# Kernel optimization log

Measured on AMD Instinct MI355X. Metric: run time of the kernel, lower is better.

## Reference

```python
import jax, jax.numpy as jnp
import numpy as np

T, H, I, E, TOPK = 4096, 2048, 2048, 16, 2

def setup_inputs() -> dict:
    key = jax.random.key(0)
    k1, k2, k3, k4 = jax.random.split(key, 4)
    return {
        "x": jax.random.normal(k1, (T, H), dtype=jnp.float32),
        "gate_w": jax.random.normal(k2, (E, H), dtype=jnp.float32) * 0.02,
        "ws": jax.random.normal(k3, (E, 2 * I, H), dtype=jnp.float32) * 0.02,
        "w2s": jax.random.normal(k4, (E, H, I), dtype=jnp.float32) * 0.02,
        "top_k": TOPK,
    }

def reference(x, gate_w, ws, w2s, top_k):
    # Router: logits -> softmax -> topk -> renormalize (top_k > 1), per fused_topk.
    logits = x @ gate_w.T                      # [T, E]
    scores = jax.nn.softmax(logits, axis=-1)
    topk_w, topk_ids = jax.lax.top_k(scores, top_k)  # [T, K]
    if top_k > 1:
        topk_w = topk_w / jnp.sum(topk_w, axis=-1, keepdims=True)
    n_exp, two_i, _ = ws.shape
    i_dim = two_i // 2

    def expert_step(acc, inp):
        w13_e, w2_e, e = inp               # [2I,H], [H,I], scalar
        gate_up = x @ w13_e.T              # [T, 2I]
        g, u = gate_up[:, :i_dim], gate_up[:, i_dim:]
        h = jax.nn.silu(g) * u             # SiluAndMul
        y = h @ w2_e.T                     # [T, H]
        coef = jnp.sum(jnp.where(topk_ids == e, topk_w, 0.0), axis=-1)  # [T]
        return acc + coef[:, None] * y, None

    init = jnp.zeros_like(x)
    eids = jnp.arange(n_exp, dtype=topk_ids.dtype)
    out, _ = jax.lax.scan(expert_step, init, (ws, w2s, eids))
    return out
```

## Files before the change

kernel.cpp:

```cpp
#include <hip/hip_runtime.h>
#include <hip/hip_bf16.h>

#define T_DIM 4096
#define H_DIM 2048
#define I_DIM 2048
#define E_NUM 16

#define BM 128
#define BN 128
#define BK 32

#define MAX_ROWS 10240

using frag_ab = __attribute__((ext_vector_type(8))) short;
using frag_cd = __attribute__((ext_vector_type(4))) float;
using ushort8 = __attribute__((ext_vector_type(8))) unsigned short;

__device__ __forceinline__ unsigned short f2bf(float f) {
    unsigned int u = __float_as_uint(f);
    u += 0x7fff + ((u >> 16) & 1);
    return (unsigned short)(u >> 16);
}
__device__ __forceinline__ float bf2f(unsigned short s) {
    return __uint_as_float(((unsigned int)s) << 16);
}

__device__ __forceinline__ void gld16(const void* g, void* l) {
    __builtin_amdgcn_global_load_lds(
        (const __attribute__((address_space(1))) unsigned int*)g,
        (__attribute__((address_space(3))) unsigned int*)l, 16, 0, 0);
}

__global__ void routing_kernel(const float* __restrict__ x,
                               const float* __restrict__ gw,
                               int* __restrict__ cnt,
                               int* __restrict__ tok_list,
                               float* __restrict__ tok_w) {
    const int wave = threadIdx.x >> 6;
    const int lane = threadIdx.x & 63;
    const int t = blockIdx.x * 4 + wave;
    if (t >= T_DIM) return;

    float acc[E_NUM];
#pragma unroll
    for (int e = 0; e < E_NUM; ++e) acc[e] = 0.f;
    const float* xr = x + (size_t)t * H_DIM;
    for (int j = lane; j < H_DIM; j += 64) {
        float xv = xr[j];
#pragma unroll
        for (int e = 0; e < E_NUM; ++e)
            acc[e] = fmaf(xv, gw[e * H_DIM + j], acc[e]);
    }
#pragma unroll
    for (int e = 0; e < E_NUM; ++e) {
        float v = acc[e];
#pragma unroll
        for (int off = 32; off > 0; off >>= 1) v += __shfl_xor(v, off);
        acc[e] = v;
    }
    if (lane == 0) {
        int b1 = 0; float l1 = acc[0];
#pragma unroll
        for (int e = 1; e < E_NUM; ++e)
            if (acc[e] > l1) { l1 = acc[e]; b1 = e; }
        int b2 = -1; float l2 = -1e30f;
#pragma unroll
        for (int e = 0; e < E_NUM; ++e)
            if (e != b1 && acc[e] > l2) { l2 = acc[e]; b2 = e; }
        float w1 = 1.f / (1.f + __expf(l2 - l1));
        float w2 = 1.f - w1;
        int p1 = atomicAdd(&cnt[b1], 1);
        tok_list[b1 * T_DIM + p1] = t; tok_w[b1 * T_DIM + p1] = w1;
        int p2 = atomicAdd(&cnt[b2], 1);
        tok_list[b2 * T_DIM + p2] = t; tok_w[b2 * T_DIM + p2] = w2;
    }
}

__global__ void scan_kernel(const int* __restrict__ cnt, int* __restrict__ base,
                            int* __restrict__ npad, int* __restrict__ total) {
    int acc = 0;
    for (int e = 0; e < E_NUM; ++e) {
        base[e] = acc;
        int p = (cnt[e] + BM - 1) & ~(BM - 1);
        npad[e] = p;
        acc += p;
    }
    *total = acc;
}

__global__ void __launch_bounds__(256) cvt_kernel(const float* __restrict__ s,
                                                  unsigned short* __restrict__ d,
                                                  size_t n8) {
    const size_t stride = (size_t)gridDim.x * 256;
    for (size_t i = (size_t)blockIdx.x * 256 + threadIdx.x; i < n8; i += stride) {
        const float4* sp = (const float4*)(s + i * 8);
        float4 a = sp[0], b = sp[1];
        ushort8 o;
        o[0] = f2bf(a.x); o[1] = f2bf(a.y); o[2] = f2bf(a.z); o[3] = f2bf(a.w);
        o[4] = f2bf(b.x); o[5] = f2bf(b.y); o[6] = f2bf(b.z); o[7] = f2bf(b.w);
        *(ushort8*)(d + i * 8) = o;
    }
}

__global__ void __launch_bounds__(256) gemm1_bf_kernel(
    const unsigned short* __restrict__ xb, const unsigned short* __restrict__ wb,
    const int* __restrict__ tok_list,
    const int* __restrict__ cnt, const int* __restrict__ base,
    const int* __restrict__ npad, unsigned short* __restrict__ gu)
{
    const int e = blockIdx.z;
    const int mt = blockIdx.y;
    if (mt * BM >= npad[e]) return;
    const int nt = blockIdx.x;

    __shared__ unsigned short As[BM * BK];
    __shared__ unsigned short Bs[BN * BK];

    const int tid = threadIdx.x;
    const int lane = tid & 63;
    const int wv = tid >> 6;
    const int wm = (wv >> 1) * 64;
    const int wn = (wv & 1) * 64;
    const int quad = lane >> 4;
    const int l16 = lane & 15;

    const int* tl = tok_list + e * T_DIM + mt * BM;
    const int lim = cnt[e] - mt * BM - 1;

    const int srow = wv * 16 + (lane >> 2);
    const int scol = (lane & 3) * 8;

    const int r0 = srow      <= lim ? srow      : lim;
    const int r1 = srow + 64 <= lim ? srow + 64 : lim;
    const unsigned short* ag0 = xb + (size_t)tl[r0] * H_DIM + scol;
    const unsigned short* ag1 = xb + (size_t)tl[r1] * H_DIM + scol;
    const unsigned short* bg0 = wb + (size_t)e * (2 * I_DIM) * H_DIM
                                   + (size_t)(nt * BN + srow) * H_DIM + scol;
    const unsigned short* bg1 = bg0 + (size_t)64 * H_DIM;

    unsigned short* al0 = &As[wv * 512];
    unsigned short* al1 = &As[2048 + wv * 512];
    unsigned short* bl0 = &Bs[wv * 512];
    unsigned short* bl1 = &Bs[2048 + wv * 512];

    frag_cd acc[4][4];
#pragma unroll
    for (int i = 0; i < 4; ++i)
#pragma unroll
        for (int j = 0; j < 4; ++j)
            acc[i][j] = (frag_cd){0.f, 0.f, 0.f, 0.f};

    for (int k0 = 0; k0 < H_DIM; k0 += BK) {
        gld16(ag0 + k0, al0);
        gld16(ag1 + k0, al1);
        gld16(bg0 + k0, bl0);
        gld16(bg1 + k0, bl1);
        __syncthreads();
        frag_ab af[4], bf[4];
#pragma unroll
        for (int i = 0; i < 4; ++i) {
            af[i] = *(const frag_ab*)(&As[(wm + i * 16 + l16) * BK + quad * 8]);
            bf[i] = *(const frag_ab*)(&Bs[(wn + i * 16 + l16) * BK + quad * 8]);
        }
#pragma unroll
        for (int i = 0; i < 4; ++i)
#pragma unroll
            for (int j = 0; j < 4; ++j)
                acc[i][j] = __builtin_amdgcn_mfma_f32_16x16x32_bf16(
                    af[i], bf[j], acc[i][j], 0, 0, 0);
        __syncthreads();
    }

    const size_t gbase = (size_t)(base[e] + mt * BM);
#pragma unroll
    for (int i = 0; i < 4; ++i) {
#pragma unroll
        for (int r = 0; r < 4; ++r) {
            int row = wm + i * 16 + quad * 4 + r;
            unsigned short* gr = gu + (gbase + row) * (size_t)(2 * I_DIM) + nt * BN + wn;
#pragma unroll
            for (int j = 0; j < 4; ++j)
                gr[j * 16 + l16] = f2bf(acc[i][j][r]);
        }
    }
}

__global__ void silu_kernel(unsigned short* __restrict__ gu,
                            const int* __restrict__ total) {
    const int tot = *total;
    size_t idx = ((size_t)blockIdx.x * 256 + threadIdx.x) * 4;
    if (idx >= (size_t)tot * I_DIM) return;
    size_t row = idx >> 11;
    int col = (int)(idx & (I_DIM - 1));
    unsigned short* gp = gu + row * (size_t)(2 * I_DIM) + col;
    ushort4 gv = *(const ushort4*)gp;
    ushort4 uv = *(const ushort4*)(gp + I_DIM);
    float g0 = bf2f(gv.x), g1 = bf2f(gv.y), g2 = bf2f(gv.z), g3 = bf2f(gv.w);
    float u0 = bf2f(uv.x), u1 = bf2f(uv.y), u2 = bf2f(uv.z), u3 = bf2f(uv.w);
    float h0 = g0 / (1.f + __expf(-g0)) * u0;
    float h1 = g1 / (1.f + __expf(-g1)) * u1;
    float h2 = g2 / (1.f + __expf(-g2)) * u2;
    float h3 = g3 / (1.f + __expf(-g3)) * u3;
    *(ushort4*)gp = make_ushort4(f2bf(h0), f2bf(h1), f2bf(h2), f2bf(h3));
}

__global__ void __launch_bounds__(256) gemm2_bf_kernel(
    const unsigned short* __restrict__ gu, const unsigned short* __restrict__ w2b,
    const int* __restrict__ tok_list, const float* __restrict__ tok_w,
    const int* __restrict__ cnt, const int* __restrict__ base,
    const int* __restrict__ npad, float* __restrict__ out)
{
    const int e = blockIdx.z;
    const int mt = blockIdx.y;
    if (mt * BM >= npad[e]) return;
    const int nt = blockIdx.x;

    __shared__ unsigned short As[BM * BK];
    __shared__ unsigned short Bs[BN * BK];
    __shared__ int s_tok[BM];
    __shared__ float s_tw[BM];

    const int tid = threadIdx.x;
    const int lane = tid & 63;
    const int wv = tid >> 6;
    const int wm = (wv >> 1) * 64;
    const int wn = (wv & 1) * 64;
    const int quad = lane >> 4;
    const int l16 = lane & 15;

    const int ne = cnt[e];
    if (tid < BM) {
        int g = mt * BM + tid;
        bool v = g < ne;
        s_tok[tid] = v ? tok_list[e * T_DIM + g] : -1;
        s_tw[tid]  = v ? tok_w[e * T_DIM + g] : 0.f;
    }

    const size_t abase = (size_t)(base[e] + mt * BM);
    const int srow = wv * 16 + (lane >> 2);
    const int scol = (lane & 3) * 8;

    const unsigned short* ag0 = gu + (abase + srow) * (size_t)(2 * I_DIM) + scol;
    const unsigned short* ag1 = ag0 + (size_t)64 * (2 * I_DIM);
    const unsigned short* bg0 = w2b + (size_t)e * H_DIM * I_DIM
                                    + (size_t)(nt * BN + srow) * I_DIM + scol;
    const unsigned short* bg1 = bg0 + (size_t)64 * I_DIM;

    unsigned short* al0 = &As[wv * 512];
    unsigned short* al1 = &As[2048 + wv * 512];
    unsigned short* bl0 = &Bs[wv * 512];
    unsigned short* bl1 = &Bs[2048 + wv * 512];

    frag_cd acc[4][4];
#pragma unroll
    for (int i = 0; i < 4; ++i)
#pragma unroll
        for (int j = 0; j < 4; ++j)
            acc[i][j] = (frag_cd){0.f, 0.f, 0.f, 0.f};

    for (int k0 = 0; k0 < I_DIM; k0 += BK) {
        gld16(ag0 + k0, al0);
        gld16(ag1 + k0, al1);
        gld16(bg0 + k0, bl0);
        gld16(bg1 + k0, bl1);
        __syncthreads();
        frag_ab af[4], bf[4];
#pragma unroll
        for (int i = 0; i < 4; ++i) {
            af[i] = *(const frag_ab*)(&As[(wm + i * 16 + l16) * BK + quad * 8]);
            bf[i] = *(const frag_ab*)(&Bs[(wn + i * 16 + l16) * BK + quad * 8]);
        }
#pragma unroll
        for (int i = 0; i < 4; ++i)
#pragma unroll
            for (int j = 0; j < 4; ++j)
                acc[i][j] = __builtin_amdgcn_mfma_f32_16x16x32_bf16(
                    af[i], bf[j], acc[i][j], 0, 0, 0);
        __syncthreads();
    }

#pragma unroll
    for (int i = 0; i < 4; ++i) {
#pragma unroll
        for (int r = 0; r < 4; ++r) {
            int row = wm + i * 16 + quad * 4 + r;
            int tok = s_tok[row];
            if (tok < 0) continue;
            float coef = s_tw[row];
            float* orow = out + (size_t)tok * H_DIM + nt * BN + wn;
#pragma unroll
            for (int j = 0; j < 4; ++j)
                atomicAdd(&orow[j * 16 + l16], coef * acc[i][j][r]);
        }
    }
}

__global__ void __launch_bounds__(256) gemm1_kernel(
    const float* __restrict__ x, const float* __restrict__ ws,
    const int* __restrict__ tok_list,
    const int* __restrict__ cnt, const int* __restrict__ base,
    const int* __restrict__ npad, unsigned short* __restrict__ gu)
{
    const int e = blockIdx.z;
    const int mt = blockIdx.y;
    if (mt * BM >= npad[e]) return;
    const int nt = blockIdx.x;

    __shared__ unsigned short As[BM * BK];
    __shared__ unsigned short Bs[BN * BK];

    const int tid = threadIdx.x;
    const int lane = tid & 63;
    const int wv = tid >> 6;
    const int wm = (wv >> 1) * 64;
    const int wn = (wv & 1) * 64;
    const int quad = lane >> 4;
    const int l16 = lane & 15;

    const int ne = cnt[e];
    const int* tl = tok_list + e * T_DIM + mt * BM;
    const int lim = ne - mt * BM - 1;

    const int ar = tid >> 3;
    const int ac = (tid & 7) * 4;

    const float* xb[4];
#pragma unroll
    for (int it = 0; it < 4; ++it) {
        int r = ar + 32 * it;
        int rr = r < lim ? r : lim;
        xb[it] = x + (size_t)tl[rr] * H_DIM + ac;
    }
    const float* w13 = ws + (size_t)e * (2 * I_DIM) * H_DIM
                          + (size_t)(nt * BN) * H_DIM + ac;

    frag_cd acc[4][4];
#pragma unroll
    for (int i = 0; i < 4; ++i)
#pragma unroll
        for (int j = 0; j < 4; ++j)
            acc[i][j] = (frag_cd){0.f, 0.f, 0.f, 0.f};

    for (int k0 = 0; k0 < H_DIM; k0 += BK) {
#pragma unroll
        for (int it = 0; it < 4; ++it) {
            int r = ar + 32 * it;
            float4 v = *(const float4*)(xb[it] + k0);
            *(ushort4*)(&As[r * BK + ac]) =
                make_ushort4(f2bf(v.x), f2bf(v.y), f2bf(v.z), f2bf(v.w));
            float4 w = *(const float4*)(w13 + (size_t)r * H_DIM + k0);
            *(ushort4*)(&Bs[r * BK + ac]) =
                make_ushort4(f2bf(w.x), f2bf(w.y), f2bf(w.z), f2bf(w.w));
        }
        __syncthreads();
        frag_ab af[4], bf[4];
#pragma unroll
        for (int i = 0; i < 4; ++i) {
            af[i] = *(const frag_ab*)(&As[(wm + i * 16 + l16) * BK + quad * 8]);
            bf[i] = *(const frag_ab*)(&Bs[(wn + i * 16 + l16) * BK + quad * 8]);
        }
#pragma unroll
        for (int i = 0; i < 4; ++i)
#pragma unroll
            for (int j = 0; j < 4; ++j)
                acc[i][j] = __builtin_amdgcn_mfma_f32_16x16x32_bf16(
                    af[i], bf[j], acc[i][j], 0, 0, 0);
        __syncthreads();
    }

    const size_t gbase = (size_t)(base[e] + mt * BM);
#pragma unroll
    for (int i = 0; i < 4; ++i) {
#pragma unroll
        for (int r = 0; r < 4; ++r) {
            int row = wm + i * 16 + quad * 4 + r;
            unsigned short* gr = gu + (gbase + row) * (size_t)(2 * I_DIM) + nt * BN + wn;
#pragma unroll
            for (int j = 0; j < 4; ++j)
                gr[j * 16 + l16] = f2bf(acc[i][j][r]);
        }
    }
}

__global__ void __launch_bounds__(256) gemm2_kernel(
    const unsigned short* __restrict__ gu, const float* __restrict__ w2s,
    const int* __restrict__ tok_list, const float* __restrict__ tok_w,
    const int* __restrict__ cnt, const int* __restrict__ base,
    const int* __restrict__ npad, float* __restrict__ out)
{
    const int e = blockIdx.z;
    const int mt = blockIdx.y;
    if (mt * BM >= npad[e]) return;
    const int nt = blockIdx.x;

    __shared__ unsigned short As[BM * BK];
    __shared__ unsigned short Bs[BN * BK];
    __shared__ int s_tok[BM];
    __shared__ float s_tw[BM];

    const int tid = threadIdx.x;
    const int lane = tid & 63;
    const int wv = tid >> 6;
    const int wm = (wv >> 1) * 64;
    const int wn = (wv & 1) * 64;
    const int quad = lane >> 4;
    const int l16 = lane & 15;

    const int ne = cnt[e];
    if (tid < BM) {
        int g = mt * BM + tid;
        bool v = g < ne;
        s_tok[tid] = v ? tok_list[e * T_DIM + g] : -1;
        s_tw[tid]  = v ? tok_w[e * T_DIM + g] : 0.f;
    }

    const size_t abase = (size_t)(base[e] + mt * BM);
    const int ar2 = tid >> 2;
    const int ac2 = (tid & 3) * 8;
    const unsigned short* ab = gu + (abase + ar2) * (size_t)(2 * I_DIM) + ac2;

    const int ar = tid >> 3;
    const int ac = (tid & 7) * 4;
    const float* w2 = w2s + (size_t)e * H_DIM * I_DIM
                          + (size_t)(nt * BN) * I_DIM + ac;

    frag_cd acc[4][4];
#pragma unroll
    for (int i = 0; i < 4; ++i)
#pragma unroll
        for (int j = 0; j < 4; ++j)
            acc[i][j] = (frag_cd){0.f, 0.f, 0.f, 0.f};

    for (int k0 = 0; k0 < I_DIM; k0 += BK) {
        *(uint4*)(&As[ar2 * BK + ac2]) = *(const uint4*)(ab + k0);
        *(uint4*)(&As[(ar2 + 64) * BK + ac2]) =
            *(const uint4*)(ab + (size_t)64 * (2 * I_DIM) + k0);
#pragma unroll
        for (int it = 0; it < 4; ++it) {
            int r = ar + 32 * it;
            float4 w = *(const float4*)(w2 + (size_t)r * I_DIM + k0);
            *(ushort4*)(&Bs[r * BK + ac]) =
                make_ushort4(f2bf(w.x), f2bf(w.y), f2bf(w.z), f2bf(w.w));
        }
        __syncthreads();
        frag_ab af[4], bf[4];
#pragma unroll
        for (int i = 0; i < 4; ++i) {
            af[i] = *(const frag_ab*)(&As[(wm + i * 16 + l16) * BK + quad * 8]);
            bf[i] = *(const frag_ab*)(&Bs[(wn + i * 16 + l16) * BK + quad * 8]);
        }
#pragma unroll
        for (int i = 0; i < 4; ++i)
#pragma unroll
            for (int j = 0; j < 4; ++j)
                acc[i][j] = __builtin_amdgcn_mfma_f32_16x16x32_bf16(
                    af[i], bf[j], acc[i][j], 0, 0, 0);
        __syncthreads();
    }

#pragma unroll
    for (int i = 0; i < 4; ++i) {
#pragma unroll
        for (int r = 0; r < 4; ++r) {
            int row = wm + i * 16 + quad * 4 + r;
            int tok = s_tok[row];
            if (tok < 0) continue;
            float coef = s_tw[row];
            float* orow = out + (size_t)tok * H_DIM + nt * BN + wn;
#pragma unroll
            for (int j = 0; j < 4; ++j)
                atomicAdd(&orow[j * 16 + l16], coef * acc[i][j][r]);
        }
    }
}

extern "C" void kernel_launch(void* const* d_in, const int* in_sizes, int n_in,
                              void* d_out, int out_size, void* d_ws, size_t ws_size,
                              hipStream_t stream) {
    const float* x   = (const float*)d_in[0];
    const float* gw  = (const float*)d_in[1];
    const float* ws  = (const float*)d_in[2];
    const float* w2s = (const float*)d_in[3];
    float* out = (float*)d_out;

    char* wsp = (char*)d_ws;
    int* cnt   = (int*)(wsp + 0);
    int* basep = (int*)(wsp + 64);
    int* npad  = (int*)(wsp + 128);
    int* total = (int*)(wsp + 192);

    const size_t MB = (size_t)1 << 20;
    const size_t NEED = 482 * MB;

    hipMemsetAsync(cnt, 0, 64, stream);
    hipMemsetAsync(d_out, 0, (size_t)T_DIM * H_DIM * sizeof(float), stream);

    if (ws_size >= NEED) {
        int*   tok_list = (int*)(wsp + 1 * MB);
        float* tok_w    = (float*)(wsp + 1 * MB + 512 * 1024);
        unsigned short* x_bf  = (unsigned short*)(wsp + 2 * MB);
        unsigned short* gu    = (unsigned short*)(wsp + 18 * MB);
        unsigned short* ws_bf = (unsigned short*)(wsp + 98 * MB);
        unsigned short* w2_bf = (unsigned short*)(wsp + 354 * MB);

        cvt_kernel<<<4096, 256, 0, stream>>>(x, x_bf, (size_t)T_DIM * H_DIM / 8);
        cvt_kernel<<<4096, 256, 0, stream>>>(ws, ws_bf,
            (size_t)E_NUM * 2 * I_DIM * H_DIM / 8);
        cvt_kernel<<<4096, 256, 0, stream>>>(w2s, w2_bf,
            (size_t)E_NUM * H_DIM * I_DIM / 8);

        routing_kernel<<<T_DIM / 4, 256, 0, stream>>>(x, gw, cnt, tok_list, tok_w);
        scan_kernel<<<1, 1, 0, stream>>>(cnt, basep, npad, total);
        gemm1_bf_kernel<<<dim3(2 * I_DIM / BN, T_DIM / BM, E_NUM), 256, 0, stream>>>(
            x_bf, ws_bf, tok_list, cnt, basep, npad, gu);
        silu_kernel<<<(MAX_ROWS * I_DIM / 4) / 256, 256, 0, stream>>>(gu, total);
        gemm2_bf_kernel<<<dim3(H_DIM / BN, T_DIM / BM, E_NUM), 256, 0, stream>>>(
            gu, w2_bf, tok_list, tok_w, cnt, basep, npad, out);
    } else {
        int*   tok_list = (int*)(wsp + 256);
        float* tok_w    = (float*)(wsp + 256 + 4 * E_NUM * T_DIM);
        unsigned short* gu = (unsigned short*)(wsp + 512 + 8 * E_NUM * T_DIM);

        routing_kernel<<<T_DIM / 4, 256, 0, stream>>>(x, gw, cnt, tok_list, tok_w);
        scan_kernel<<<1, 1, 0, stream>>>(cnt, basep, npad, total);
        gemm1_kernel<<<dim3(2 * I_DIM / BN, T_DIM / BM, E_NUM), 256, 0, stream>>>(
            x, ws, tok_list, cnt, basep, npad, gu);
        silu_kernel<<<(MAX_ROWS * I_DIM / 4) / 256, 256, 0, stream>>>(gu, total);
        gemm2_kernel<<<dim3(H_DIM / BN, T_DIM / BM, E_NUM), 256, 0, stream>>>(
            gu, w2s, tok_list, tok_w, cnt, basep, npad, out);
    }
}
```

Baseline: 1.431 ms.

## Convert fp32 weights to bf16 inside GEMMs with double-buffered LDS and compact tile grid

Drops the separate conversion passes over both expert weight tensors. The GEMMs now read fp32 weights directly, pack them to bf16 in registers and store them into a double-buffered LDS tile while the current tile's MFMAs run. A scan kernel also builds a compact list of (expert, m-tile) pairs, so the grid only launches live tiles instead of a mostly empty E×T/BM grid. This removes a full fp32 read plus bf16 write and re-read of about 0.5 GB of weights, but each GEMM block re-reads fp32 weights for every m-tile (twice the bytes of bf16), and converts in VALU on the critical path.

```diff
diff --git a/kernel.cpp b/kernel.cpp
--- a/kernel.cpp
+++ b/kernel.cpp
@@ -11,6 +11,7 @@
 #define BK 32
 
 #define MAX_ROWS 10240
+#define MAX_TILES 80
 
 using frag_ab = __attribute__((ext_vector_type(8))) short;
 using frag_cd = __attribute__((ext_vector_type(4))) float;
@@ -23,6 +24,13 @@
 }
 __device__ __forceinline__ float bf2f(unsigned short s) {
     return __uint_as_float(((unsigned int)s) << 16);
+}
+
+__device__ __forceinline__ unsigned int pk2(float a, float b) {
+    __hip_bfloat162 h = __float22bfloat162_rn(make_float2(a, b));
+    union { __hip_bfloat162 h2; unsigned int u; } c;
+    c.h2 = h;
+    return c.u;
 }
 
 __device__ __forceinline__ void gld16(const void* g, void* l) {
@@ -86,6 +94,27 @@
         acc += p;
     }
     *total = acc;
+}
+
+__global__ void scan_tiles_kernel(const int* __restrict__ cnt,
+                                  int* __restrict__ base,
+                                  int* __restrict__ npad,
+                                  int* __restrict__ total,
+                                  int* __restrict__ ntile,
+                                  int* __restrict__ te,
+                                  int* __restrict__ tmt) {
+    int acc = 0, nt = 0;
+    for (int e = 0; e < E_NUM; ++e) {
+        base[e] = acc;
+        int p = (cnt[e] + BM - 1) & ~(BM - 1);
+        npad[e] = p;
+        acc += p;
+        for (int m = 0; m * BM < p && nt < MAX_TILES; ++m) {
+            te[nt] = e; tmt[nt] = m; ++nt;
+        }
+    }
+    *total = acc;
+    *ntile = nt;
 }
 
 __global__ void __launch_bounds__(256) cvt_kernel(const float* __restrict__ s,
@@ -102,19 +131,21 @@
     }
 }
 
-__global__ void __launch_bounds__(256) gemm1_bf_kernel(
-    const unsigned short* __restrict__ xb, const unsigned short* __restrict__ wb,
-    const int* __restrict__ tok_list,
-    const int* __restrict__ cnt, const int* __restrict__ base,
-    const int* __restrict__ npad, unsigned short* __restrict__ gu)
+__global__ void __launch_bounds__(256) gemm1_hyb_kernel(
+    const unsigned short* __restrict__ xb, const float* __restrict__ ws,
+    const int* __restrict__ tok_list, const int* __restrict__ cnt,
+    const int* __restrict__ base, const int* __restrict__ ntile,
+    const int* __restrict__ te, const int* __restrict__ tmt,
+    unsigned short* __restrict__ gu)
 {
-    const int e = blockIdx.z;
-    const int mt = blockIdx.y;
-    if (mt * BM >= npad[e]) return;
+    const int ty = blockIdx.y;
+    if (ty >= *ntile) return;
+    const int e  = te[ty];
+    const int mt = tmt[ty];
     const int nt = blockIdx.x;
 
-    __shared__ unsigned short As[BM * BK];
-    __shared__ unsigned short Bs[BN * BK];
+    __shared__ unsigned short As[2 * BM * BK];
+    __shared__ unsigned short Bs[2 * BN * BK];
 
     const int tid = threadIdx.x;
     const int lane = tid & 63;
@@ -129,19 +160,15 @@
 
     const int srow = wv * 16 + (lane >> 2);
     const int scol = (lane & 3) * 8;
-
     const int r0 = srow      <= lim ? srow      : lim;
     const int r1 = srow + 64 <= lim ? srow + 64 : lim;
     const unsigned short* ag0 = xb + (size_t)tl[r0] * H_DIM + scol;
     const unsigned short* ag1 = xb + (size_t)tl[r1] * H_DIM + scol;
-    const unsigned short* bg0 = wb + (size_t)e * (2 * I_DIM) * H_DIM
-                                   + (size_t)(nt * BN + srow) * H_DIM + scol;
-    const unsigned short* bg1 = bg0 + (size_t)64 * H_DIM;
-
-    unsigned short* al0 = &As[wv * 512];
-    unsigned short* al1 = &As[2048 + wv * 512];
-    unsigned short* bl0 = &Bs[wv * 512];
-    unsigned short* bl1 = &Bs[2048 + wv * 512];
+
+    const int br = tid >> 3;
+    const int bc = (tid & 7) * 4;
+    const float* wsb = ws + (size_t)e * (2 * I_DIM) * H_DIM
+                          + (size_t)(nt * BN + br) * H_DIM + bc;
 
     frag_cd acc[4][4];
 #pragma unroll
@@ -150,25 +177,52 @@
         for (int j = 0; j < 4; ++j)
             acc[i][j] = (frag_cd){0.f, 0.f, 0.f, 0.f};
 
+    {
+        float4 w0[4];
+#pragma unroll
+        for (int it = 0; it < 4; ++it)
+            w0[it] = *(const float4*)(wsb + (size_t)(32 * it) * H_DIM);
+        gld16(ag0, &As[wv * 512]);
+        gld16(ag1, &As[2048 + wv * 512]);
+#pragma unroll
+        for (int it = 0; it < 4; ++it)
+            *(uint2*)(&Bs[(br + 32 * it) * BK + bc]) =
+                make_uint2(pk2(w0[it].x, w0[it].y), pk2(w0[it].z, w0[it].w));
+    }
+    __syncthreads();
+
+    int cur = 0;
     for (int k0 = 0; k0 < H_DIM; k0 += BK) {
-        gld16(ag0 + k0, al0);
-        gld16(ag1 + k0, al1);
-        gld16(bg0 + k0, bl0);
-        gld16(bg1 + k0, bl1);
+        const int nxt = cur ^ 1;
+        const bool pf = (k0 + BK) < H_DIM;
+        float4 wreg[4];
+        if (pf) {
+#pragma unroll
+            for (int it = 0; it < 4; ++it)
+                wreg[it] = *(const float4*)(wsb + (size_t)(32 * it) * H_DIM + k0 + BK);
+            gld16(ag0 + k0 + BK, &As[nxt * 4096 + wv * 512]);
+            gld16(ag1 + k0 + BK, &As[nxt * 4096 + 2048 + wv * 512]);
+        }
+        frag_ab af[4], bfr[4];
+#pragma unroll
+        for (int i = 0; i < 4; ++i) {
+            af[i]  = *(const frag_ab*)(&As[cur * 4096 + (wm + i * 16 + l16) * BK + quad * 8]);
+            bfr[i] = *(const frag_ab*)(&Bs[cur * 4096 + (wn + i * 16 + l16) * BK + quad * 8]);
+        }
+#pragma unroll
+        for (int i = 0; i < 4; ++i)
+#pragma unroll
+            for (int j = 0; j < 4; ++j)
+                acc[i][j] = __builtin_amdgcn_mfma_f32_16x16x32_bf16(
+                    af[i], bfr[j], acc[i][j], 0, 0, 0);
+        if (pf) {
+#pragma unroll
+            for (int it = 0; it < 4; ++it)
+                *(uint2*)(&Bs[nxt * 4096 + (br + 32 * it) * BK + bc]) =
+                    make_uint2(pk2(wreg[it].x, wreg[it].y), pk2(wreg[it].z, wreg[it].w));
+        }
         __syncthreads();
-        frag_ab af[4], bf[4];
-#pragma unroll
-        for (int i = 0; i < 4; ++i) {
-            af[i] = *(const frag_ab*)(&As[(wm + i * 16 + l16) * BK + quad * 8]);
-            bf[i] = *(const frag_ab*)(&Bs[(wn + i * 16 + l16) * BK + quad * 8]);
-        }
-#pragma unroll
-        for (int i = 0; i < 4; ++i)
-#pragma unroll
-            for (int j = 0; j < 4; ++j)
-                acc[i][j] = __builtin_amdgcn_mfma_f32_16x16x32_bf16(
-                    af[i], bf[j], acc[i][j], 0, 0, 0);
-        __syncthreads();
+        cur = nxt;
     }
 
     const size_t gbase = (size_t)(base[e] + mt * BM);
@@ -204,19 +258,21 @@
     *(ushort4*)gp = make_ushort4(f2bf(h0), f2bf(h1), f2bf(h2), f2bf(h3));
 }
 
-__global__ void __launch_bounds__(256) gemm2_bf_kernel(
-    const unsigned short* __restrict__ gu, const unsigned short* __restrict__ w2b,
+__global__ void __launch_bounds__(256) gemm2_hyb_kernel(
+    const unsigned short* __restrict__ gu, const float* __restrict__ w2s,
     const int* __restrict__ tok_list, const float* __restrict__ tok_w,
     const int* __restrict__ cnt, const int* __restrict__ base,
-    const int* __restrict__ npad, float* __restrict__ out)
+    const int* __restrict__ ntile, const int* __restrict__ te,
+    const int* __restrict__ tmt, float* __restrict__ out)
 {
-    const int e = blockIdx.z;
-    const int mt = blockIdx.y;
-    if (mt * BM >= npad[e]) return;
+    const int ty = blockIdx.y;
+    if (ty >= *ntile) return;
+    const int e  = te[ty];
+    const int mt = tmt[ty];
     const int nt = blockIdx.x;
 
-    __shared__ unsigned short As[BM * BK];
-    __shared__ unsigned short Bs[BN * BK];
+    __shared__ unsigned short As[2 * BM * BK];
+    __shared__ unsigned short Bs[2 * BN * BK];
     __shared__ int s_tok[BM];
     __shared__ float s_tw[BM];
 
@@ -239,17 +295,13 @@
     const size_t abase = (size_t)(base[e] + mt * BM);
     const int srow = wv * 16 + (lane >> 2);
     const int scol = (lane & 3) * 8;
-
     const unsigned short* ag0 = gu + (abase + srow) * (size_t)(2 * I_DIM) + scol;
     const unsigned short* ag1 = ag0 + (size_t)64 * (2 * I_DIM);
-    const unsigned short* bg0 = w2b + (size_t)e * H_DIM * I_DIM
-                                    + (size_t)(nt * BN + srow) * I_DIM + scol;
-    const unsigned short* bg1 = bg0 + (size_t)64 * I_DIM;
-
-    unsigned short* al0 = &As[wv * 512];
-    unsigned short* al1 = &As[2048 + wv * 512];
-    unsigned short* bl0 = &Bs[wv * 512];
-    unsigned short* bl1 = &Bs[2048 + wv * 512];
+
+    const int br = tid >> 3;
+    const int bc = (tid & 7) * 4;
+    const float* w2b = w2s + (size_t)e * H_DIM * I_DIM
+                           + (size_t)(nt * BN + br) * I_DIM + bc;
 
     frag_cd acc[4][4];
 #pragma unroll
@@ -258,25 +310,52 @@
         for (int j = 0; j < 4; ++j)
             acc[i][j] = (frag_cd){0.f, 0.f, 0.f, 0.f};
 
+    {
+        float4 w0[4];
+#pragma unroll
+        for (int it = 0; it < 4; ++it)
+            w0[it] = *(const float4*)(w2b + (size_t)(32 * it) * I_DIM);
+        gld16(ag0, &As[wv * 512]);
+        gld16(ag1, &As[2048 + wv * 512]);
+#pragma unroll
+        for (int it = 0; it < 4; ++it)
+            *(uint2*)(&Bs[(br + 32 * it) * BK + bc]) =
+                make_uint2(pk2(w0[it].x, w0[it].y), pk2(w0[it].z, w0[it].w));
+    }
+    __syncthreads();
+
+    int cur = 0;
     for (int k0 = 0; k0 < I_DIM; k0 += BK) {
-        gld16(ag0 + k0, al0);
-        gld16(ag1 + k0, al1);
-        gld16(bg0 + k0, bl0);
-        gld16(bg1 + k0, bl1);
+        const int nxt = cur ^ 1;
+        const bool pf = (k0 + BK) < I_DIM;
+        float4 wreg[4];
+        if (pf) {
+#pragma unroll
+            for (int it = 0; it < 4; ++it)
+                wreg[it] = *(const float4*)(w2b + (size_t)(32 * it) * I_DIM + k0 + BK);
+            gld16(ag0 + k0 + BK, &As[nxt * 4096 + wv * 512]);
+            gld16(ag1 + k0 + BK, &As[nxt * 4096 + 2048 + wv * 512]);
+        }
+        frag_ab af[4], bfr[4];
+#pragma unroll
+        for (int i = 0; i < 4; ++i) {
+            af[i]  = *(const frag_ab*)(&As[cur * 4096 + (wm + i * 16 + l16) * BK + quad * 8]);
+            bfr[i] = *(const frag_ab*)(&Bs[cur * 4096 + (wn + i * 16 + l16) * BK + quad * 8]);
+        }
+#pragma unroll
+        for (int i = 0; i < 4; ++i)
+#pragma unroll
+            for (int j = 0; j < 4; ++j)
+                acc[i][j] = __builtin_amdgcn_mfma_f32_16x16x32_bf16(
+                    af[i], bfr[j], acc[i][j], 0, 0, 0);
+        if (pf) {
+#pragma unroll
+            for (int it = 0; it < 4; ++it)
+                *(uint2*)(&Bs[nxt * 4096 + (br + 32 * it) * BK + bc]) =
+                    make_uint2(pk2(wreg[it].x, wreg[it].y), pk2(wreg[it].z, wreg[it].w));
+        }
         __syncthreads();
-        frag_ab af[4], bf[4];
-#pragma unroll
-        for (int i = 0; i < 4; ++i) {
-            af[i] = *(const frag_ab*)(&As[(wm + i * 16 + l16) * BK + quad * 8]);
-            bf[i] = *(const frag_ab*)(&Bs[(wn + i * 16 + l16) * BK + quad * 8]);
-        }
-#pragma unroll
-        for (int i = 0; i < 4; ++i)
-#pragma unroll
-            for (int j = 0; j < 4; ++j)
-                acc[i][j] = __builtin_amdgcn_mfma_f32_16x16x32_bf16(
-                    af[i], bf[j], acc[i][j], 0, 0, 0);
-        __syncthreads();
+        cur = nxt;
     }
 
 #pragma unroll
@@ -490,32 +569,29 @@
     int* total = (int*)(wsp + 192);
 
     const size_t MB = (size_t)1 << 20;
-    const size_t NEED = 482 * MB;
+    const size_t NEED = 100 * MB;
 
     hipMemsetAsync(cnt, 0, 64, stream);
     hipMemsetAsync(d_out, 0, (size_t)T_DIM * H_DIM * sizeof(float), stream);
 
     if (ws_size >= NEED) {
+        int* ntile = (int*)(wsp + 256);
+        int* te    = (int*)(wsp + 512);
+        int* tmt   = (int*)(wsp + 1024);
         int*   tok_list = (int*)(wsp + 1 * MB);
         float* tok_w    = (float*)(wsp + 1 * MB + 512 * 1024);
-        unsigned short* x_bf  = (unsigned short*)(wsp + 2 * MB);
-        unsigned short* gu    = (unsigned short*)(wsp + 18 * MB);
-        unsigned short* ws_bf = (unsigned short*)(wsp + 98 * MB);
-        unsigned short* w2_bf = (unsigned short*)(wsp + 354 * MB);
-
-        cvt_kernel<<<4096, 256, 0, stream>>>(x, x_bf, (size_t)T_DIM * H_DIM / 8);
-        cvt_kernel<<<4096, 256, 0, stream>>>(ws, ws_bf,
-            (size_t)E_NUM * 2 * I_DIM * H_DIM / 8);
-        cvt_kernel<<<4096, 256, 0, stream>>>(w2s, w2_bf,
-            (size_t)E_NUM * H_DIM * I_DIM / 8);
-
+        unsigned short* x_bf = (unsigned short*)(wsp + 2 * MB);
+        unsigned short* gu   = (unsigned short*)(wsp + 18 * MB);
+
+        cvt_kernel<<<2048, 256, 0, stream>>>(x, x_bf, (size_t)T_DIM * H_DIM / 8);
         routing_kernel<<<T_DIM / 4, 256, 0, stream>>>(x, gw, cnt, tok_list, tok_w);
-        scan_kernel<<<1, 1, 0, stream>>>(cnt, basep, npad, total);
-        gemm1_bf_kernel<<<dim3(2 * I_DIM / BN, T_DIM / BM, E_NUM), 256, 0, stream>>>(
-            x_bf, ws_bf, tok_list, cnt, basep, npad, gu);
+        scan_tiles_kernel<<<1, 1, 0, stream>>>(cnt, basep, npad, total,
+                                               ntile, te, tmt);
+        gemm1_hyb_kernel<<<dim3(2 * I_DIM / BN, MAX_TILES), 256, 0, stream>>>(
+            x_bf, ws, tok_list, cnt, basep, ntile, te, tmt, gu);
         silu_kernel<<<(MAX_ROWS * I_DIM / 4) / 256, 256, 0, stream>>>(gu, total);
-        gemm2_bf_kernel<<<dim3(H_DIM / BN, T_DIM / BM, E_NUM), 256, 0, stream>>>(
-            gu, w2_bf, tok_list, tok_w, cnt, basep, npad, out);
+        gemm2_hyb_kernel<<<dim3(H_DIM / BN, MAX_TILES), 256, 0, stream>>>(
+            gu, w2s, tok_list, tok_w, cnt, basep, ntile, te, tmt, out);
     } else {
         int*   tok_list = (int*)(wsp + 256);
         float* tok_w    = (float*)(wsp + 256 + 4 * E_NUM * T_DIM);
```

After: 1.452 ms. Within noise of the previous version (+1.5%).
